# Performance work log

Hardware: AMD Instinct MI355X
Metric: run time of the kernel (lower is better)

## Reference

```python
import jax, jax.numpy as jnp
import numpy as np

DMODEL = 1024
DK = 64
DHEAD = 16
DEPTH = DK * DHEAD
N, LQ, L = 4, 4096, 4096
FAC1 = 1.0 / np.sqrt(DK)  # relu kernel scale folded into omega, as in reset()
EPS = 1e-6


def setup_inputs() -> dict:
    key = jax.random.key(0)
    ks = jax.random.split(key, 10)
    x = jax.random.normal(ks[0], (N, LQ, DMODEL), jnp.float32)
    y = jax.random.normal(ks[1], (N, L, DMODEL), jnp.float32)
    s_in = 1.0 / np.sqrt(DMODEL)
    s_depth = 1.0 / np.sqrt(DEPTH)
    # Linear weights stored as (in, out) so application is x @ W + b
    WQ = jax.random.normal(ks[2], (DMODEL, DEPTH), jnp.float32) * s_in
    WK = jax.random.normal(ks[3], (DMODEL, DEPTH), jnp.float32) * s_in
    WV = jax.random.normal(ks[4], (DMODEL, DEPTH), jnp.float32) * s_in
    WO = jax.random.normal(ks[5], (DEPTH, DMODEL), jnp.float32) * s_depth
    bQ = jnp.zeros((DEPTH,), jnp.float32)
    bK = jnp.zeros((DEPTH,), jnp.float32)
    bV = jnp.zeros((DEPTH,), jnp.float32)
    bO = jnp.zeros((DMODEL,), jnp.float32)
    # orthogonal random-feature projection: QR of gaussian, scaled by sqrt(dk), then *fac1 (relu)
    g = np.random.default_rng(0).standard_normal((DK, DK)).astype(np.float32)
    qmat, _ = np.linalg.qr(g)
    omega = jnp.asarray(qmat * np.sqrt(DK) * FAC1, dtype=jnp.float32)
    return dict(x=x, y=y, WQ=WQ, bQ=bQ, WK=WK, bK=bK, WV=WV, bV=bV,
                WO=WO, bO=bO, omega=omega)


def reference(x, y, WQ, bQ, WK, bK, WV, bV, WO, bO, omega):
    n, lq, _ = x.shape
    l = y.shape[1]
    # project and split heads: (n, h, L, dk)
    q = (x @ WQ + bQ).reshape(n, lq, DHEAD, DK).transpose(0, 2, 1, 3)
    k = (y @ WK + bK).reshape(n, l, DHEAD, DK).transpose(0, 2, 1, 3)
    v = (y @ WV + bV).reshape(n, l, DHEAD, DK).transpose(0, 2, 1, 3)
    # relu random-feature map phi(x) = relu(x @ omega) + eps
    q = jax.nn.relu(q @ omega) + EPS
    k = jax.nn.relu(k @ omega) + EPS
    # linear attention: out = phi(q) @ (phi(k)^T @ v) / (phi(q) @ phi(k)^T @ 1)
    kv = jnp.einsum('nhld,nhle->nhde', k, v)          # (n, h, dk, dk)
    ksum = jnp.sum(k, axis=2)                          # (n, h, dk)
    d_inv = jnp.einsum('nhqd,nhd->nhq', q, ksum)[..., None]
    out = jnp.einsum('nhqd,nhde->nhqe', q, kv) / d_inv  # (n, h, Lq, dk)
    out = out.transpose(0, 2, 1, 3).reshape(n, lq, DEPTH)
    return out @ WO + bO
```

## Files before the change

### kernel.cpp

```cpp
#include <hip/hip_runtime.h>

#define EPSF 1e-6f

typedef _Float16 f16x8 __attribute__((ext_vector_type(8)));
typedef _Float16 f16x4 __attribute__((ext_vector_type(4)));
typedef float    f32x4 __attribute__((ext_vector_type(4)));

#define GLL16(gp, lp) __builtin_amdgcn_global_load_lds( \
    (const __attribute__((address_space(1))) void*)(gp), \
    (__attribute__((address_space(3))) void*)(lp), 16, 0, 0)

__global__ __launch_bounds__(256) void cvt2_f16(const float* __restrict__ inA,
                                                _Float16* __restrict__ outA,
                                                const float* __restrict__ inB,
                                                _Float16* __restrict__ outB, int n8each) {
    int idx = blockIdx.x * 256 + threadIdx.x;
    const float* in = inA; _Float16* out = outA;
    if (idx >= n8each) { idx -= n8each; in = inB; out = outB; }
    const float4* p = (const float4*)in + (size_t)idx * 2;
    float4 a = p[0], b = p[1];
    f16x8 o;
    o[0] = (_Float16)a.x; o[1] = (_Float16)a.y; o[2] = (_Float16)a.z; o[3] = (_Float16)a.w;
    o[4] = (_Float16)b.x; o[5] = (_Float16)b.y; o[6] = (_Float16)b.z; o[7] = (_Float16)b.w;
    *(f16x8*)(out + (size_t)idx * 8) = o;
}

__global__ __launch_bounds__(256) void prep_all(const float* __restrict__ omega,
                                                const float* __restrict__ bQ,
                                                const float* __restrict__ bK,
                                                const float* __restrict__ bV,
                                                _Float16* __restrict__ obdT,
                                                float* __restrict__ bQf,
                                                float* __restrict__ bkv,
                                                float* __restrict__ ksum) {
    int idx = blockIdx.x * 256 + threadIdx.x;
    int c = idx >> 10, k = idx & 1023;
    float v = ((c >> 6) == (k >> 6)) ? omega[(k & 63) * 64 + (c & 63)] : 0.f;
    obdT[idx] = (_Float16)v;
    if (idx < 4096) ksum[idx] = 0.f;
    if (idx < 1024) {
        int h = idx >> 6, e = idx & 63;
        float sq = 0.f, sk = 0.f;
        for (int d = 0; d < 64; d++) {
            float o = omega[d * 64 + e];
            sq += bQ[h * 64 + d] * o;
            sk += bK[h * 64 + d] * o;
        }
        bQf[idx] = sq;
        bkv[idx] = sk;
        bkv[1024 + idx] = bV[idx];
    }
}

__global__ __launch_bounds__(256) void transpose_cvt(const float* __restrict__ in,
                                                     _Float16* __restrict__ out) {
    __shared__ float tile[64][65];
    const int t = threadIdx.x;
    const int k0 = blockIdx.x * 64, n0 = blockIdx.y * 64;
#pragma unroll
    for (int j = 0; j < 16; j++) {
        int idx = j * 256 + t; int r = idx >> 6, c = idx & 63;
        tile[r][c] = in[(size_t)(k0 + r) * 1024 + n0 + c];
    }
    __syncthreads();
#pragma unroll
    for (int j = 0; j < 16; j++) {
        int idx = j * 256 + t; int rn = idx >> 6, ck = idx & 63;
        out[(size_t)(n0 + rn) * 1024 + k0 + ck] = (_Float16)tile[ck][rn];
    }
}

__global__ __launch_bounds__(256) void gemm_fold(const _Float16* __restrict__ A,
                                                 const _Float16* __restrict__ Bt,
                                                 _Float16* __restrict__ out0,
                                                 _Float16* __restrict__ out1) {
    const int K = 1024;
    __shared__ __align__(16) _Float16 Asm[128 * 32];
    __shared__ __align__(16) _Float16 Bsm[128 * 32];
    const int t = threadIdx.x, lane = t & 63, w = t >> 6;
    const int bm = blockIdx.y * 128, bn = blockIdx.x * 128;
    const int wm = (w >> 1) * 64, wn = (w & 1) * 64;
    const int r15 = lane & 15, slog = lane >> 4;

    int aoff[4], boff[4];
#pragma unroll
    for (int m = 0; m < 4; m++) {
        int ra = wm + m * 16 + r15;
        aoff[m] = ra * 32 + (slog ^ ((ra >> 1) & 3)) * 8;
        int rb = wn + m * 16 + r15;
        boff[m] = rb * 32 + (slog ^ ((rb >> 1) & 3)) * 8;
    }
    f32x4 acc[4][4];
#pragma unroll
    for (int m = 0; m < 4; m++)
#pragma unroll
        for (int n = 0; n < 4; n++) acc[m][n] = (f32x4){0.f, 0.f, 0.f, 0.f};

    for (int kt = 0; kt < K; kt += 32) {
        __syncthreads();
#pragma unroll
        for (int i = 0; i < 2; i++) {
            int seg = i * 256 + w * 64 + lane;
            int r = seg >> 2, sp = seg & 3;
            int sg = sp ^ ((r >> 1) & 3);
            GLL16(A  + (size_t)(bm + r) * K + kt + sg * 8, Asm + (size_t)(i * 256 + w * 64) * 8);
            GLL16(Bt + (size_t)(bn + r) * K + kt + sg * 8, Bsm + (size_t)(i * 256 + w * 64) * 8);
        }
        __syncthreads();
        f16x8 av[4], bv[4];
#pragma unroll
        for (int m = 0; m < 4; m++) av[m] = *(const f16x8*)(Asm + aoff[m]);
#pragma unroll
        for (int n = 0; n < 4; n++) bv[n] = *(const f16x8*)(Bsm + boff[n]);
#pragma unroll
        for (int m = 0; m < 4; m++)
#pragma unroll
            for (int n = 0; n < 4; n++)
                acc[m][n] = __builtin_amdgcn_mfma_f32_16x16x32_f16(av[m], bv[n], acc[m][n], 0, 0, 0);
    }

#pragma unroll
    for (int m = 0; m < 4; m++) {
        int row0 = bm + wm + m * 16 + slog * 4;
        _Float16* C = (row0 < 1024) ? out0 : out1;
        int l = row0 & 1023;
#pragma unroll
        for (int n = 0; n < 4; n++) {
            int colg = bn + wn + n * 16 + r15;
            f16x4 p;
#pragma unroll
            for (int j = 0; j < 4; j++) p[j] = (_Float16)acc[m][n][j];
            *(f16x4*)(C + (size_t)colg * 1024 + l) = p;
        }
    }
}

template<int EPI>
__global__ __launch_bounds__(512, 2) void gemm256(const _Float16* __restrict__ A,
                                                  const _Float16* __restrict__ Bt,
                                                  const float* __restrict__ bias,
                                                  void* __restrict__ out0,
                                                  void* __restrict__ out1,
                                                  float* __restrict__ ksum,
                                                  int M, int N, int K, int nbn) {
    __shared__ __align__(16) char lds[131072];
    const int t = threadIdx.x, lane = t & 63, w = t >> 6;
    const int nwg = gridDim.x;
    const int f = (blockIdx.x & 7) * (nwg >> 3) + (blockIdx.x >> 3);
    const int bm = (f / nbn) * 256, bn = (f % nbn) * 256;
    const int wm = (w & 1) * 128, wn = (w >> 1) * 64;
    const int r15 = lane & 15, hi = lane >> 4;
    const int srow = lane >> 2, sp = lane & 3;
    const _Float16* BtU = (EPI == 2) ? Bt + ((size_t)(bm >> 12) << 20) : Bt;

    int aoff[8], boff[4];
#pragma unroll
    for (int m = 0; m < 8; m++) {
        int r = wm + m * 16 + r15;
        aoff[m] = r * 64 + (((hi + (r >> 1)) & 3) << 4);
    }
#pragma unroll
    for (int n = 0; n < 4; n++) {
        int r = wn + n * 16 + r15;
        boff[n] = r * 64 + (((hi + (r >> 1)) & 3) << 4);
    }

    f32x4 acc[8][4];
#pragma unroll
    for (int m = 0; m < 8; m++)
#pragma unroll
        for (int n = 0; n < 4; n++) acc[m][n] = (f32x4){0.f, 0.f, 0.f, 0.f};

    auto stage = [&](int s) {
        char* base = lds + (s & 3) * 32768;
        int kt = s * 32;
#pragma unroll
        for (int p = 0; p < 2; p++) {
            int row = w * 32 + p * 16 + srow;
            int sg = (sp - ((row >> 1) & 3)) & 3;
            GLL16(A   + (size_t)(bm + row) * K + kt + sg * 8, base + w * 2048 + p * 1024);
            GLL16(BtU + (size_t)(bn + row) * K + kt + sg * 8, base + 16384 + w * 2048 + p * 1024);
        }
    };

    const int NS = K >> 5;
    stage(0); stage(1); stage(2);
    for (int s = 0; s < NS; ++s) {
        if (s + 2 < NS)      asm volatile("s_waitcnt vmcnt(8)" ::: "memory");
        else if (s + 1 < NS) asm volatile("s_waitcnt vmcnt(4)" ::: "memory");
        else                 asm volatile("s_waitcnt vmcnt(0)" ::: "memory");
        asm volatile("s_barrier" ::: "memory");
        if (s + 3 < NS) stage(s + 3);
        const char* La = lds + (s & 3) * 32768;
        const char* Lb = La + 16384;
        f16x8 bv[4];
#pragma unroll
        for (int n = 0; n < 4; n++) bv[n] = *(const f16x8*)(Lb + boff[n]);
        f16x8 av[8];
#pragma unroll
        for (int m = 0; m < 8; m++) av[m] = *(const f16x8*)(La + aoff[m]);
        __builtin_amdgcn_s_setprio(1);
#pragma unroll
        for (int m = 0; m < 8; m++)
#pragma unroll
            for (int n = 0; n < 4; n++)
                acc[m][n] = __builtin_amdgcn_mfma_f32_16x16x32_f16(av[m], bv[n], acc[m][n], 0, 0, 0);
        __builtin_amdgcn_s_setprio(0);
    }

    if (EPI == 3) {
        asm volatile("s_barrier" ::: "memory");
        char* LW = lds + w * 16384;
        const int colg0 = bn + wn;
        const bool isK = colg0 < 1024;
        _Float16* Cb = isK ? (_Float16*)out0 : (_Float16*)out1;
        const int hd = (isK ? colg0 : colg0 - 1024) >> 6;
        const int nb = bm >> 12;
        const int l0 = (bm & 4095) + wm;
        float cs[4] = {0.f, 0.f, 0.f, 0.f};
#pragma unroll
        for (int m = 0; m < 8; m++)
#pragma unroll
            for (int n = 0; n < 4; n++) {
                int d = n * 16 + r15;
                float bs = bias[colg0 + d];
                f16x4 pk;
#pragma unroll
                for (int j = 0; j < 4; j++) {
                    float xv = acc[m][n][j] + bs;
                    if (isK) { xv = fmaxf(xv, 0.f) + EPSF; cs[n] += xv; }
                    pk[j] = (_Float16)xv;
                }
                *(f16x4*)(LW + d * 256 + ((m * 32 + hi * 8) ^ ((d & 15) << 4))) = pk;
            }
        if (isK) {
#pragma unroll
            for (int n = 0; n < 4; n++) {
                cs[n] += __shfl_xor(cs[n], 16, 64);
                cs[n] += __shfl_xor(cs[n], 32, 64);
            }
            if (hi == 0) {
#pragma unroll
                for (int n = 0; n < 4; n++)
                    atomicAdd(ksum + (size_t)(nb * 16 + hd) * 64 + n * 16 + r15, cs[n]);
            }
        }
        _Float16* basep = Cb + (size_t)(nb * 16 + hd) * 64 * 4096 + l0;
#pragma unroll
        for (int pass = 0; pass < 16; pass++) {
            int d = pass * 4 + hi;
            f16x8 v = *(const f16x8*)(LW + d * 256 + ((r15 * 16) ^ ((d & 15) << 4)));
            *(f16x8*)(basep + (size_t)d * 4096 + r15 * 8) = v;
        }
    } else if (EPI == 4) {
        const int headg = (bm >> 12) * 16 + ((bn + wn) >> 6);
        const float* ks = (const float*)out1;
        float ksn[4];
#pragma unroll
        for (int n = 0; n < 4; n++) ksn[n] = ks[(size_t)headg * 64 + n * 16 + r15];
        _Float16* C = (_Float16*)out0;
#pragma unroll
        for (int m = 0; m < 8; m++) {
            int row0 = bm + wm + m * 16 + hi * 4;
            float qv[4][4], dp[4] = {0.f, 0.f, 0.f, 0.f};
#pragma unroll
            for (int n = 0; n < 4; n++) {
                int colg = bn + wn + n * 16 + r15;
                float bs = bias[colg];
#pragma unroll
                for (int j = 0; j < 4; j++) {
                    float xv = fmaxf(acc[m][n][j] + bs, 0.f) + EPSF;
                    qv[n][j] = xv;
                    dp[j] += xv * ksn[n];
                }
            }
#pragma unroll
            for (int j = 0; j < 4; j++) {
                dp[j] += __shfl_xor(dp[j], 1, 64);
                dp[j] += __shfl_xor(dp[j], 2, 64);
                dp[j] += __shfl_xor(dp[j], 4, 64);
                dp[j] += __shfl_xor(dp[j], 8, 64);
                dp[j] = 4096.0f * __builtin_amdgcn_rcpf(dp[j]);
            }
#pragma unroll
            for (int n = 0; n < 4; n++) {
                int colg = bn + wn + n * 16 + r15;
#pragma unroll
                for (int j = 0; j < 4; j++)
                    C[(size_t)(row0 + j) * N + colg] = (_Float16)(qv[n][j] * dp[j]);
            }
        }
    } else {
#pragma unroll
        for (int m = 0; m < 8; m++) {
            int row0 = bm + wm + m * 16 + hi * 4;
#pragma unroll
            for (int n = 0; n < 4; n++) {
                int colg = bn + wn + n * 16 + r15;
                float bs = bias ? bias[colg] : 0.f;
#pragma unroll
                for (int j = 0; j < 4; j++)
                    ((float*)out0)[(size_t)(row0 + j) * N + colg] = acc[m][n][j] + bs;
            }
        }
    }
}

__global__ __launch_bounds__(256) void kvt_kernel(const _Float16* __restrict__ Vt,
                                                  const _Float16* __restrict__ KphiT,
                                                  float* __restrict__ kvpart) {
    const int t = threadIdx.x, lane = t & 63, w = t >> 6;
    const int head = blockIdx.y;
    const int l0 = blockIdx.x * 1024;
    __shared__ __align__(16) _Float16 As[64 * 128];
    __shared__ __align__(16) _Float16 Bs[64 * 128];
    const int r15 = lane & 15, slog = lane >> 4;
    f32x4 acc[4][4];
#pragma unroll
    for (int m = 0; m < 4; m++)
#pragma unroll
        for (int n = 0; n < 4; n++) acc[m][n] = (f32x4){0.f, 0.f, 0.f, 0.f};

    for (int it = 0; it < 8; it++) {
        __syncthreads();
        int lbase = l0 + it * 128;
#pragma unroll
        for (int i = 0; i < 4; i++) {
            int seg = i * 256 + w * 64 + lane;
            int r = seg >> 4, sp2 = seg & 15;
            int sg = sp2 ^ (r & 15);
            GLL16(Vt    + ((size_t)head * 64 + r) * 4096 + lbase + sg * 8, As + (size_t)(i * 256 + w * 64) * 8);
            GLL16(KphiT + ((size_t)head * 64 + r) * 4096 + lbase + sg * 8, Bs + (size_t)(i * 256 + w * 64) * 8);
        }
        __syncthreads();
        f16x8 av[4], bv[4];
#pragma unroll
        for (int m = 0; m < 4; m++) {
            int r = m * 16 + r15;
            int s2 = w * 4 + slog;
            int ph = s2 ^ (r & 15);
            av[m] = *(const f16x8*)(As + r * 128 + ph * 8);
            bv[m] = *(const f16x8*)(Bs + r * 128 + ph * 8);
        }
#pragma unroll
        for (int m = 0; m < 4; m++)
#pragma unroll
            for (int n = 0; n < 4; n++)
                acc[m][n] = __builtin_amdgcn_mfma_f32_16x16x32_f16(av[m], bv[n], acc[m][n], 0, 0, 0);
    }
    float* red = (float*)As;
    for (int ww = 0; ww < 4; ww++) {
        __syncthreads();
        if (w == ww) {
#pragma unroll
            for (int m = 0; m < 4; m++)
#pragma unroll
                for (int n = 0; n < 4; n++)
#pragma unroll
                    for (int j = 0; j < 4; j++) {
                        int row = m * 16 + slog * 4 + j, col = n * 16 + r15;
                        if (ww == 0) red[row * 64 + col] = acc[m][n][j];
                        else         red[row * 64 + col] += acc[m][n][j];
                    }
        }
    }
    __syncthreads();
    float* outp = kvpart + ((size_t)head * 4 + blockIdx.x) * 4096;
#pragma unroll
    for (int i = 0; i < 16; i++) { int idx = i * 256 + t; outp[idx] = red[idx]; }
}

__global__ __launch_bounds__(256) void w2t_kernel(const _Float16* __restrict__ Wot,
                                                  const float* __restrict__ kvpart,
                                                  _Float16* __restrict__ W2t) {
    const int t = threadIdx.x;
    const int jb = blockIdx.x;
    const int gh = blockIdx.y;
    const int b = gh >> 4, hl = gh & 15;
    __shared__ float kvL[64][65];
    const float* kp = kvpart + (size_t)gh * 4 * 4096;
#pragma unroll
    for (int i = 0; i < 16; i++) {
        int idx = i * 256 + t;
        float s = 0.f;
#pragma unroll
        for (int c = 0; c < 4; c++) s += kp[c * 4096 + idx];
        kvL[idx >> 6][idx & 63] = s;
    }
    __syncthreads();
    const int j = jb * 128 + (t >> 1);
    const int d0 = (t & 1) * 32;
    const _Float16* wr = Wot + (size_t)j * 1024 + hl * 64;
    float wv[64];
#pragma unroll
    for (int i = 0; i < 8; i++) {
        f16x8 v = *(const f16x8*)(wr + i * 8);
#pragma unroll
        for (int k = 0; k < 8; k++) wv[i * 8 + k] = (float)v[k];
    }
    _Float16* outp = W2t + ((size_t)b << 20) + (size_t)j * 1024 + hl * 64 + d0;
#pragma unroll
    for (int d = 0; d < 32; d++) {
        float s = 0.f;
#pragma unroll
        for (int e = 0; e < 64; e++) s += wv[e] * kvL[e][d0 + d];
        outp[d] = (_Float16)(s * (1.0f / 4096.0f));
    }
}

extern "C" void kernel_launch(void* const* d_in, const int* in_sizes, int n_in,
                              void* d_out, int out_size, void* d_ws, size_t ws_size,
                              hipStream_t stream) {
    (void)in_sizes; (void)n_in; (void)out_size; (void)ws_size;
    const float* x     = (const float*)d_in[0];
    const float* y     = (const float*)d_in[1];
    const float* WQ    = (const float*)d_in[2];
    const float* bQ    = (const float*)d_in[3];
    const float* WK    = (const float*)d_in[4];
    const float* bK    = (const float*)d_in[5];
    const float* WV    = (const float*)d_in[6];
    const float* bV    = (const float*)d_in[7];
    const float* WO    = (const float*)d_in[8];
    const float* bO    = (const float*)d_in[9];
    const float* omega = (const float*)d_in[10];

    char* ws = (char*)d_ws;
    size_t off = 0;
    auto alloc = [&](size_t bytes) { void* p = ws + off; off += (bytes + 255) & ~(size_t)255; return p; };
    const size_t BIG = (size_t)16384 * 1024 * 2;
    _Float16* xb    = (_Float16*)alloc(BIG);
    _Float16* yb    = (_Float16*)alloc(BIG);
    _Float16* WQKb  = (_Float16*)alloc((size_t)2048 * 1024 * 2);
    _Float16* obdT  = (_Float16*)alloc(1024 * 1024 * 2);
    _Float16* Wqt   = (_Float16*)alloc(1024 * 1024 * 2);
    _Float16* Wkvt  = (_Float16*)alloc((size_t)2048 * 1024 * 2);
    _Float16* Wot   = (_Float16*)alloc(1024 * 1024 * 2);
    _Float16* W2t   = (_Float16*)alloc((size_t)4 * 1024 * 1024 * 2);
    float*    bQf   = (float*)alloc(1024 * 4);
    float*    bkv   = (float*)alloc(2048 * 4);
    _Float16* U2    = (_Float16*)alloc(BIG);
    _Float16* KphiT = (_Float16*)alloc(BIG);
    _Float16* Vt    = (_Float16*)alloc(BIG);
    float*    kvpart= (float*)alloc((size_t)256 * 4096 * 4);
    float*    ksum  = (float*)alloc((size_t)64 * 64 * 4);

    cvt2_f16<<<16384, 256, 0, stream>>>(x, xb, y, yb, 16384 * 1024 / 8);
    cvt2_f16<<<1024, 256, 0, stream>>>(WQ, WQKb, WK, WQKb + (size_t)1024 * 1024, 1024 * 1024 / 8);
    prep_all<<<4096, 256, 0, stream>>>(omega, bQ, bK, bV, obdT, bQf, bkv, ksum);
    transpose_cvt<<<dim3(16, 16), 256, 0, stream>>>(WV, Wkvt + (size_t)1024 * 1024);
    transpose_cvt<<<dim3(16, 16), 256, 0, stream>>>(WO, Wot);
    gemm_fold<<<dim3(8, 16), 256, 0, stream>>>(WQKb, obdT, Wqt, Wkvt);
    gemm256<3><<<512, 512, 0, stream>>>(yb, Wkvt, bkv, KphiT, Vt, ksum, 16384, 2048, 1024, 8);
    kvt_kernel<<<dim3(4, 64), 256, 0, stream>>>(Vt, KphiT, kvpart);
    w2t_kernel<<<dim3(8, 64), 256, 0, stream>>>(Wot, kvpart, W2t);
    gemm256<4><<<256, 512, 0, stream>>>(xb, Wqt, bQf, U2, ksum, nullptr, 16384, 1024, 1024, 4);
    gemm256<2><<<256, 512, 0, stream>>>(U2, W2t, bO, d_out, nullptr, nullptr, 16384, 1024, 1024, 4);
}
```

Before: 280.2 us.

## Fuse K^T V reduction into the K/V projection GEMM epilogue

Interleaves the K and V weight columns per head so that each 256-wide output tile of the projection GEMM holds matching K and V for two heads. The epilogue stages phi(K) and V in LDS and computes per-tile partial K^T V products with MFMA, writing 16 partials per head. A small reduction kernel then sums them, which removes the round trip of writing and re-reading the full transposed K and V tensors (about 64 MB of f16). The cost is a heavier epilogue with extra LDS traffic and MFMA work, and a larger partial buffer to reduce.

Result: faster. 261.3 us (-6.7%).

```diff
diff --git a/kernel.cpp b/kernel.cpp
--- a/kernel.cpp
+++ b/kernel.cpp
@@ -47,13 +47,13 @@
             sk += bK[h * 64 + d] * o;
         }
         bQf[idx] = sq;
-        bkv[idx] = sk;
-        bkv[1024 + idx] = bV[idx];
+        bkv[h * 128 + e] = sk;
+        bkv[h * 128 + 64 + e] = bV[idx];
     }
 }
 
 __global__ __launch_bounds__(256) void transpose_cvt(const float* __restrict__ in,
-                                                     _Float16* __restrict__ out) {
+                                                     _Float16* __restrict__ out, int vmode) {
     __shared__ float tile[64][65];
     const int t = threadIdx.x;
     const int k0 = blockIdx.x * 64, n0 = blockIdx.y * 64;
@@ -66,7 +66,9 @@
 #pragma unroll
     for (int j = 0; j < 16; j++) {
         int idx = j * 256 + t; int rn = idx >> 6, ck = idx & 63;
-        out[(size_t)(n0 + rn) * 1024 + k0 + ck] = (_Float16)tile[ck][rn];
+        int rowo = n0 + rn;
+        if (vmode) rowo = ((rowo >> 6) << 7) + 64 + (rowo & 63);
+        out[(size_t)rowo * 1024 + k0 + ck] = (_Float16)tile[ck][rn];
     }
 }
 
@@ -122,7 +124,6 @@
 #pragma unroll
     for (int m = 0; m < 4; m++) {
         int row0 = bm + wm + m * 16 + slog * 4;
-        _Float16* C = (row0 < 1024) ? out0 : out1;
         int l = row0 & 1023;
 #pragma unroll
         for (int n = 0; n < 4; n++) {
@@ -130,7 +131,12 @@
             f16x4 p;
 #pragma unroll
             for (int j = 0; j < 4; j++) p[j] = (_Float16)acc[m][n][j];
-            *(f16x4*)(C + (size_t)colg * 1024 + l) = p;
+            if (row0 < 1024) {
+                *(f16x4*)(out0 + (size_t)colg * 1024 + l) = p;
+            } else {
+                int rr = ((colg >> 6) << 7) + (colg & 63);
+                *(f16x4*)(out1 + (size_t)rr * 1024 + l) = p;
+            }
         }
     }
 }
@@ -208,22 +214,20 @@
         __builtin_amdgcn_s_setprio(0);
     }
 
-    if (EPI == 3) {
-        asm volatile("s_barrier" ::: "memory");
-        char* LW = lds + w * 16384;
-        const int colg0 = bn + wn;
-        const bool isK = colg0 < 1024;
-        _Float16* Cb = isK ? (_Float16*)out0 : (_Float16*)out1;
-        const int hd = (isK ? colg0 : colg0 - 1024) >> 6;
+    if (EPI == 5) {
+        const int q = w >> 1;
+        const bool isK = !(q & 1);
         const int nb = bm >> 12;
-        const int l0 = (bm & 4095) + wm;
+        const int g0 = bn >> 7;
+        __syncthreads();
+        char* LT = lds + q * 32768;
         float cs[4] = {0.f, 0.f, 0.f, 0.f};
 #pragma unroll
         for (int m = 0; m < 8; m++)
 #pragma unroll
             for (int n = 0; n < 4; n++) {
-                int d = n * 16 + r15;
-                float bs = bias[colg0 + d];
+                int dd = n * 16 + r15;
+                float bs = bias[bn + wn + dd];
                 f16x4 pk;
 #pragma unroll
                 for (int j = 0; j < 4; j++) {
@@ -231,7 +235,8 @@
                     if (isK) { xv = fmaxf(xv, 0.f) + EPSF; cs[n] += xv; }
                     pk[j] = (_Float16)xv;
                 }
-                *(f16x4*)(LW + d * 256 + ((m * 32 + hi * 8) ^ ((d & 15) << 4))) = pk;
+                int l2 = (wm + m * 16 + hi * 4) * 2;
+                *(f16x4*)(LT + dd * 512 + (l2 ^ ((dd & 7) << 4))) = pk;
             }
         if (isK) {
 #pragma unroll
@@ -242,15 +247,38 @@
             if (hi == 0) {
 #pragma unroll
                 for (int n = 0; n < 4; n++)
-                    atomicAdd(ksum + (size_t)(nb * 16 + hd) * 64 + n * 16 + r15, cs[n]);
-            }
-        }
-        _Float16* basep = Cb + (size_t)(nb * 16 + hd) * 64 * 4096 + l0;
-#pragma unroll
-        for (int pass = 0; pass < 16; pass++) {
-            int d = pass * 4 + hi;
-            f16x8 v = *(const f16x8*)(LW + d * 256 + ((r15 * 16) ^ ((d & 15) << 4)));
-            *(f16x8*)(basep + (size_t)d * 4096 + r15 * 8) = v;
+                    atomicAdd(ksum + (size_t)(nb * 16 + g0 + (q >> 1)) * 64 + n * 16 + r15, cs[n]);
+            }
+        }
+        __syncthreads();
+        f32x4 kva[4];
+#pragma unroll
+        for (int i = 0; i < 4; i++) kva[i] = (f32x4){0.f, 0.f, 0.f, 0.f};
+#pragma unroll
+        for (int i = 0; i < 4; i++) {
+            int tt = w * 4 + i;
+            int hl = tt >> 4, dg = (tt >> 2) & 3, eg = tt & 3;
+            const char* KT = lds + (hl * 2) * 32768;
+            const char* VT = lds + (hl * 2 + 1) * 32768;
+            int d = dg * 16 + r15, e = eg * 16 + r15;
+#pragma unroll
+            for (int ks = 0; ks < 8; ks++) {
+                int l2 = (ks * 32 + hi * 8) * 2;
+                f16x8 ka = *(const f16x8*)(KT + d * 512 + (l2 ^ ((d & 7) << 4)));
+                f16x8 vb = *(const f16x8*)(VT + e * 512 + (l2 ^ ((e & 7) << 4)));
+                kva[i] = __builtin_amdgcn_mfma_f32_16x16x32_f16(ka, vb, kva[i], 0, 0, 0);
+            }
+        }
+        const int chunk = (bm >> 8) & 15;
+        float* kvp = (float*)out0;
+#pragma unroll
+        for (int i = 0; i < 4; i++) {
+            int tt = w * 4 + i;
+            int hl = tt >> 4, dg = (tt >> 2) & 3, eg = tt & 3;
+            float* dst = kvp + ((size_t)(nb * 16 + g0 + hl) * 16 + chunk) * 4096;
+#pragma unroll
+            for (int j = 0; j < 4; j++)
+                dst[(dg * 16 + hi * 4 + j) * 64 + eg * 16 + r15] = kva[i][j];
         }
     } else if (EPI == 4) {
         const int headg = (bm >> 12) * 16 + ((bn + wn) >> 6);
@@ -306,86 +334,33 @@
     }
 }
 
-__global__ __launch_bounds__(256) void kvt_kernel(const _Float16* __restrict__ Vt,
-                                                  const _Float16* __restrict__ KphiT,
-                                                  float* __restrict__ kvpart) {
-    const int t = threadIdx.x, lane = t & 63, w = t >> 6;
-    const int head = blockIdx.y;
-    const int l0 = blockIdx.x * 1024;
-    __shared__ __align__(16) _Float16 As[64 * 128];
-    __shared__ __align__(16) _Float16 Bs[64 * 128];
-    const int r15 = lane & 15, slog = lane >> 4;
-    f32x4 acc[4][4];
-#pragma unroll
-    for (int m = 0; m < 4; m++)
-#pragma unroll
-        for (int n = 0; n < 4; n++) acc[m][n] = (f32x4){0.f, 0.f, 0.f, 0.f};
-
-    for (int it = 0; it < 8; it++) {
-        __syncthreads();
-        int lbase = l0 + it * 128;
-#pragma unroll
-        for (int i = 0; i < 4; i++) {
-            int seg = i * 256 + w * 64 + lane;
-            int r = seg >> 4, sp2 = seg & 15;
-            int sg = sp2 ^ (r & 15);
-            GLL16(Vt    + ((size_t)head * 64 + r) * 4096 + lbase + sg * 8, As + (size_t)(i * 256 + w * 64) * 8);
-            GLL16(KphiT + ((size_t)head * 64 + r) * 4096 + lbase + sg * 8, Bs + (size_t)(i * 256 + w * 64) * 8);
-        }
-        __syncthreads();
-        f16x8 av[4], bv[4];
-#pragma unroll
-        for (int m = 0; m < 4; m++) {
-            int r = m * 16 + r15;
-            int s2 = w * 4 + slog;
-            int ph = s2 ^ (r & 15);
-            av[m] = *(const f16x8*)(As + r * 128 + ph * 8);
-            bv[m] = *(const f16x8*)(Bs + r * 128 + ph * 8);
-        }
-#pragma unroll
-        for (int m = 0; m < 4; m++)
-#pragma unroll
-            for (int n = 0; n < 4; n++)
-                acc[m][n] = __builtin_amdgcn_mfma_f32_16x16x32_f16(av[m], bv[n], acc[m][n], 0, 0, 0);
-    }
-    float* red = (float*)As;
-    for (int ww = 0; ww < 4; ww++) {
-        __syncthreads();
-        if (w == ww) {
-#pragma unroll
-            for (int m = 0; m < 4; m++)
-#pragma unroll
-                for (int n = 0; n < 4; n++)
-#pragma unroll
-                    for (int j = 0; j < 4; j++) {
-                        int row = m * 16 + slog * 4 + j, col = n * 16 + r15;
-                        if (ww == 0) red[row * 64 + col] = acc[m][n][j];
-                        else         red[row * 64 + col] += acc[m][n][j];
-                    }
-        }
-    }
-    __syncthreads();
-    float* outp = kvpart + ((size_t)head * 4 + blockIdx.x) * 4096;
-#pragma unroll
-    for (int i = 0; i < 16; i++) { int idx = i * 256 + t; outp[idx] = red[idx]; }
+__global__ __launch_bounds__(256) void kvred16(const float* __restrict__ kvpart,
+                                               float* __restrict__ kvT) {
+    int gh = blockIdx.x, t = threadIdx.x;
+    const float* kp = kvpart + (size_t)gh * 16 * 4096;
+#pragma unroll
+    for (int i = 0; i < 16; i++) {
+        int idx = i * 256 + t;
+        float s = 0.f;
+#pragma unroll
+        for (int c = 0; c < 16; c++) s += kp[c * 4096 + idx];
+        kvT[(size_t)gh * 4096 + idx] = s;
+    }
 }
 
 __global__ __launch_bounds__(256) void w2t_kernel(const _Float16* __restrict__ Wot,
-                                                  const float* __restrict__ kvpart,
+                                                  const float* __restrict__ kvT,
                                                   _Float16* __restrict__ W2t) {
     const int t = threadIdx.x;
     const int jb = blockIdx.x;
     const int gh = blockIdx.y;
     const int b = gh >> 4, hl = gh & 15;
     __shared__ float kvL[64][65];
-    const float* kp = kvpart + (size_t)gh * 4 * 4096;
+    const float* kp = kvT + (size_t)gh * 4096;
 #pragma unroll
     for (int i = 0; i < 16; i++) {
         int idx = i * 256 + t;
-        float s = 0.f;
-#pragma unroll
-        for (int c = 0; c < 4; c++) s += kp[c * 4096 + idx];
-        kvL[idx >> 6][idx & 63] = s;
+        kvL[idx & 63][idx >> 6] = kp[idx];
     }
     __syncthreads();
     const int j = jb * 128 + (t >> 1);
@@ -439,20 +414,19 @@
     float*    bQf   = (float*)alloc(1024 * 4);
     float*    bkv   = (float*)alloc(2048 * 4);
     _Float16* U2    = (_Float16*)alloc(BIG);
-    _Float16* KphiT = (_Float16*)alloc(BIG);
-    _Float16* Vt    = (_Float16*)alloc(BIG);
-    float*    kvpart= (float*)alloc((size_t)256 * 4096 * 4);
+    float*    kvpart= (float*)alloc((size_t)64 * 16 * 4096 * 4);
+    float*    kvT   = (float*)alloc((size_t)64 * 4096 * 4);
     float*    ksum  = (float*)alloc((size_t)64 * 64 * 4);
 
     cvt2_f16<<<16384, 256, 0, stream>>>(x, xb, y, yb, 16384 * 1024 / 8);
     cvt2_f16<<<1024, 256, 0, stream>>>(WQ, WQKb, WK, WQKb + (size_t)1024 * 1024, 1024 * 1024 / 8);
     prep_all<<<4096, 256, 0, stream>>>(omega, bQ, bK, bV, obdT, bQf, bkv, ksum);
-    transpose_cvt<<<dim3(16, 16), 256, 0, stream>>>(WV, Wkvt + (size_t)1024 * 1024);
-    transpose_cvt<<<dim3(16, 16), 256, 0, stream>>>(WO, Wot);
+    transpose_cvt<<<dim3(16, 16), 256, 0, stream>>>(WV, Wkvt, 1);
+    transpose_cvt<<<dim3(16, 16), 256, 0, stream>>>(WO, Wot, 0);
     gemm_fold<<<dim3(8, 16), 256, 0, stream>>>(WQKb, obdT, Wqt, Wkvt);
-    gemm256<3><<<512, 512, 0, stream>>>(yb, Wkvt, bkv, KphiT, Vt, ksum, 16384, 2048, 1024, 8);
-    kvt_kernel<<<dim3(4, 64), 256, 0, stream>>>(Vt, KphiT, kvpart);
-    w2t_kernel<<<dim3(8, 64), 256, 0, stream>>>(Wot, kvpart, W2t);
+    gemm256<5><<<512, 512, 0, stream>>>(yb, Wkvt, bkv, kvpart, nullptr, ksum, 16384, 2048, 1024, 8);
+    kvred16<<<64, 256, 0, stream>>>(kvpart, kvT);
+    w2t_kernel<<<dim3(8, 64), 256, 0, stream>>>(Wot, kvT, W2t);
     gemm256<4><<<256, 512, 0, stream>>>(xb, Wqt, bQf, U2, ksum, nullptr, 16384, 1024, 1024, 4);
     gemm256<2><<<256, 512, 0, stream>>>(U2, W2t, bO, d_out, nullptr, nullptr, 16384, 1024, 1024, 4);
 }
```
